# Kernel tuning notes

Measured on AMD Instinct MI355X. Metric: run time of the kernel, lower is better.

## Reference

```python
import jax, jax.numpy as jnp
import numpy as np

N, E, IN, ED, HID, HEADS, OUT, G = 50000, 800000, 128, 16, 32, 4, 64, 64
NEG_SLOPE = 0.2


def gat_conv(x, src, dst, edge_attr, W, att_src, att_dst, We, att_edge, bias,
             heads, out_ch, concat):
    """PyG-style GATConv with edge attributes and mean-filled self loops.
    src/dst already include self loops; edge_attr already includes fill rows."""
    n = x.shape[0]
    h = (x @ W).reshape(n, heads, out_ch)                      # [N,H,C]
    a_src = jnp.einsum('nhc,hc->nh', h, att_src)               # [N,H]
    a_dst = jnp.einsum('nhc,hc->nh', h, att_dst)
    eh = (edge_attr @ We).reshape(-1, heads, out_ch)           # [E',H,C]
    a_edge = jnp.einsum('ehc,hc->eh', eh, att_edge)            # [E',H]
    alpha = jax.nn.leaky_relu(a_src[src] + a_dst[dst] + a_edge, NEG_SLOPE)
    # segment softmax over incoming edges of each target node
    amax = jax.ops.segment_max(alpha, dst, num_segments=n)
    ex = jnp.exp(alpha - amax[dst])
    denom = jax.ops.segment_sum(ex, dst, num_segments=n)
    coef = ex / (denom[dst] + 1e-16)                           # [E',H]
    msg = h[src] * coef[:, :, None]                            # [E',H,C]
    out = jax.ops.segment_sum(msg, dst, num_segments=n)        # [N,H,C]
    out = out.reshape(n, heads * out_ch) if concat else out.mean(axis=1)
    return out + bias


def add_self_loops(edge_index, edge_attr, n):
    loop = jnp.arange(n, dtype=edge_index.dtype)
    src = jnp.concatenate([edge_index[0], loop])
    dst = jnp.concatenate([edge_index[1], loop])
    fill = jnp.broadcast_to(edge_attr.mean(axis=0), (n, edge_attr.shape[1]))
    ea = jnp.concatenate([edge_attr, fill], axis=0)
    return src, dst, ea


def setup_inputs() -> dict:
    key = jax.random.key(0)
    ks = jax.random.split(key, 16)
    s1 = 1.0 / np.sqrt(IN)
    s2 = 1.0 / np.sqrt(HID * HEADS)
    se = 1.0 / np.sqrt(ED)
    return {
        'x': jax.random.normal(ks[0], (N, IN), jnp.float32),
        'edge_index': jax.random.randint(ks[1], (2, E), 0, N, jnp.int64),
        'edge_attr': jax.random.normal(ks[2], (E, ED), jnp.float32),
        'batch': jnp.sort(jax.random.randint(ks[3], (N,), 0, G, jnp.int64)),
        # layer 1 params (heads=4, concat=True)
        'W1': jax.random.normal(ks[4], (IN, HEADS * HID), jnp.float32) * s1,
        'att_src1': jax.random.normal(ks[5], (HEADS, HID), jnp.float32) * s1,
        'att_dst1': jax.random.normal(ks[6], (HEADS, HID), jnp.float32) * s1,
        'We1': jax.random.normal(ks[7], (ED, HEADS * HID), jnp.float32) * se,
        'att_edge1': jax.random.normal(ks[8], (HEADS, HID), jnp.float32) * se,
        'b1': jnp.zeros((HEADS * HID,), jnp.float32),
        # layer 2 params (heads=1, concat=False)
        'W2': jax.random.normal(ks[9], (HEADS * HID, OUT), jnp.float32) * s2,
        'att_src2': jax.random.normal(ks[10], (1, OUT), jnp.float32) * s2,
        'att_dst2': jax.random.normal(ks[11], (1, OUT), jnp.float32) * s2,
        'We2': jax.random.normal(ks[12], (ED, OUT), jnp.float32) * se,
        'att_edge2': jax.random.normal(ks[13], (1, OUT), jnp.float32) * se,
        'b2': jnp.zeros((OUT,), jnp.float32),
    }


def reference(x, edge_index, edge_attr, batch,
              W1, att_src1, att_dst1, We1, att_edge1, b1,
              W2, att_src2, att_dst2, We2, att_edge2, b2):
    src, dst, ea = add_self_loops(edge_index, edge_attr, x.shape[0])
    h = gat_conv(x, src, dst, ea, W1, att_src1, att_dst1, We1, att_edge1, b1,
                 HEADS, HID, concat=True)
    h = jax.nn.elu(h)
    h = gat_conv(h, src, dst, ea, W2, att_src2, att_dst2, We2, att_edge2, b2,
                 1, OUT, concat=False)
    # global mean pool over graphs
    sums = jax.ops.segment_sum(h, batch, num_segments=G)
    cnts = jax.ops.segment_sum(jnp.ones((h.shape[0],), h.dtype), batch, num_segments=G)
    return sums / jnp.maximum(cnts, 1.0)[:, None]
```

## Files before the change

### kernel.cpp

```cpp
#include <hip/hip_runtime.h>
#include <hip/hip_fp16.h>
#include <math.h>

#define NN 50000
#define NE 800000
#define EDF 16
#define C1 128
#define HID 32
#define OUTF 64
#define NG 64
#define SLOPE 0.2f
#define CAP 64
#define PB 256
#define PCH 196
#define HB 3125
#define PRB 125
#define G2B 1563
#define FB 4688
#define ZTOT 54104
#define ZB 212
#define WZB 309

static inline int cdiv(long a, long b){ return (int)((a + b - 1) / b); }

__device__ __forceinline__ float lrelu(float x){ return x >= 0.f ? x : SLOPE * x; }

typedef _Float16 f16x8 __attribute__((ext_vector_type(8)));
typedef float f32x4 __attribute__((ext_vector_type(4)));
#define MFMA16(a, b, c) __builtin_amdgcn_mfma_f32_16x16x32_f16((a), (b), (c), 0, 0, 0)

__global__ __launch_bounds__(256) void k_wsplit(
    const float* __restrict__ W1, const float* __restrict__ W2,
    __half* __restrict__ W1Th, __half* __restrict__ W1Tl,
    __half* __restrict__ W2Th, __half* __restrict__ W2Tl,
    int* __restrict__ zbase,
    const float* __restrict__ We1, const float* __restrict__ att_e1,
    const float* __restrict__ We2, const float* __restrict__ att_e2,
    float* __restrict__ M1g, float* __restrict__ M2g){
  int t = threadIdx.x;
  int bid = blockIdx.x;
  if (bid < 64){
    int i = bid * 256 + t;
    int c = i & 127, k = i >> 7;
    float w = W1[i];
    __half h = __float2half_rn(w);
    W1Th[c * 128 + k] = h;
    W1Tl[c * 128 + k] = __float2half_rn((w - __half2float(h)) * 4096.0f);
    return;
  }
  if (bid < 96){
    int i = (bid - 64) * 256 + t;
    int c = i & 63, k = i >> 6;
    float w = W2[i];
    __half h = __float2half_rn(w);
    W2Th[c * 128 + k] = h;
    W2Tl[c * 128 + k] = __float2half_rn((w - __half2float(h)) * 4096.0f);
    return;
  }
  if (bid < 96 + ZB){
    int i = (bid - 96) * 256 + t;
    if (i < ZTOT) zbase[i] = 0;
    return;
  }
  if (t < 64){
    int h = t >> 4, d = t & 15;
    float s = 0.f;
    for (int c = 0; c < HID; c++) s += We1[d * C1 + h * HID + c] * att_e1[h * HID + c];
    M1g[t] = s;
  }
  if (t >= 64 && t < 80){
    int d = t - 64;
    float s = 0.f;
    for (int c = 0; c < OUTF; c++) s += We2[d * OUTF + c] * att_e2[c];
    M2g[d] = s;
  }
}

__global__ __launch_bounds__(256) void k_fuse(
    const float* __restrict__ ea,
    const int* __restrict__ src, const int* __restrict__ dst,
    const float* __restrict__ M1g, const float* __restrict__ M2g,
    int* __restrict__ deg, unsigned int* __restrict__ recC,
    float* __restrict__ part,
    const float* __restrict__ x,
    const __half* __restrict__ W1Th, const __half* __restrict__ W1Tl,
    __half* __restrict__ Ch,
    const float* __restrict__ attS, const float* __restrict__ attD,
    float* __restrict__ aS, float* __restrict__ aD){
  __shared__ __align__(16) __half Ash[4096];
  __shared__ __align__(16) __half Asl[4096];
  __shared__ float sM[80];
  __shared__ float sWS[64];
  int t = threadIdx.x;
  int bid = blockIdx.x;
  int rem = bid % 3;
  if (rem != 0){
    int pb = (bid / 3) * 2 + (rem - 1);
    if (t < 80) sM[t] = (t < 64) ? M1g[t] : M2g[t - 64];
    __syncthreads();
    long e = (long)pb * 256 + t;
    float eav[16];
    const float4* p = (const float4*)(ea + e * EDF);
    *(float4*)&eav[0]  = p[0]; *(float4*)&eav[4]  = p[1];
    *(float4*)&eav[8]  = p[2]; *(float4*)&eav[12] = p[3];
    int s = src[e];
    int d = dst[e];
    unsigned rk = (unsigned)atomicAdd(&deg[d], 1);
    float ae[4];
#pragma unroll
    for (int h = 0; h < 4; h++){
      float sdot = 0.f;
#pragma unroll
      for (int dd = 0; dd < 16; dd++) sdot += eav[dd] * sM[h * 16 + dd];
      ae[h] = sdot;
    }
    float a2 = 0.f;
#pragma unroll
    for (int dd = 0; dd < 16; dd++) a2 += eav[dd] * sM[64 + dd];
    __half2 ae01 = __floats2half2_rn(ae[0], ae[1]);
    __half2 ae23 = __floats2half2_rn(ae[2], ae[3]);
    __half  a2h  = __float2half_rn(a2);
    uint4 rec;
    rec.x = (unsigned)s | ((unsigned)*(unsigned short*)&a2h << 16);
    rec.y = *(unsigned*)&ae01;
    rec.z = *(unsigned*)&ae23;
    rec.w = 0u;
    *(uint4*)&recC[((long)d * CAP + rk) * 4] = rec;
    int lane = t & 63, wid = t >> 6;
#pragma unroll
    for (int c = 0; c < 16; c++){
      float v = eav[c];
#pragma unroll
      for (int off = 32; off > 0; off >>= 1) v += __shfl_xor(v, off);
      if (lane == 0) sWS[wid * 16 + c] = v;
    }
    __syncthreads();
    if (t < 16)
      part[pb * 16 + t] = sWS[t] + sWS[16 + t] + sWS[32 + t] + sWS[48 + t];
    return;
  }
  int row0 = (bid / 3) * 32;
  {
    int srow = t >> 3, sseg = t & 7;
    int gr = row0 + srow;
    float xv[16];
    if (gr < NN){
      const float4* xp = (const float4*)(x + (long)gr * 128 + sseg * 16);
      *(float4*)&xv[0]  = xp[0]; *(float4*)&xv[4]  = xp[1];
      *(float4*)&xv[8]  = xp[2]; *(float4*)&xv[12] = xp[3];
    } else {
#pragma unroll
      for (int i = 0; i < 16; i++) xv[i] = 0.f;
    }
    f16x8 vh[2], vl[2];
#pragma unroll
    for (int q = 0; q < 2; q++)
#pragma unroll
      for (int i = 0; i < 8; i++){
        float f = xv[q * 8 + i];
        _Float16 h = (_Float16)f;
        vh[q][i] = h;
        vl[q][i] = (_Float16)(f - (float)h);
      }
    int sb = srow * 256 + sseg * 32;
    int sw = (srow & 7) << 4;
    *(f16x8*)((char*)Ash + ((sb     ) ^ sw)) = vh[0];
    *(f16x8*)((char*)Ash + ((sb + 16) ^ sw)) = vh[1];
    *(f16x8*)((char*)Asl + ((sb     ) ^ sw)) = vl[0];
    *(f16x8*)((char*)Asl + ((sb + 16) ^ sw)) = vl[1];
  }
  __syncthreads();
  int wave = t >> 6, lane = t & 63, g = lane >> 4, li = lane & 15;
  const f16x8* BhP = (const f16x8*)W1Th;
  const f16x8* BlP = (const f16x8*)W1Tl;
  int c0 = wave * 32 + li;
  int c1 = c0 + 16;
  f32x4 z = {0.f, 0.f, 0.f, 0.f};
  f32x4 aM00 = z, aM01 = z, aM10 = z, aM11 = z;
  f32x4 aL00 = z, aL01 = z, aL10 = z, aL11 = z;
  int ro0 = li * 256, ro1 = (16 + li) * 256;
  int sw0 = (li & 7) << 4;
#pragma unroll
  for (int ks = 0; ks < 4; ks++){
    int ko = ks * 64 + g * 16;
    f16x8 ah0 = *(const f16x8*)((char*)Ash + ((ro0 + ko) ^ sw0));
    f16x8 ah1 = *(const f16x8*)((char*)Ash + ((ro1 + ko) ^ sw0));
    f16x8 al0 = *(const f16x8*)((char*)Asl + ((ro0 + ko) ^ sw0));
    f16x8 al1 = *(const f16x8*)((char*)Asl + ((ro1 + ko) ^ sw0));
    f16x8 bh0 = BhP[c0 * 16 + ks * 4 + g];
    f16x8 bh1 = BhP[c1 * 16 + ks * 4 + g];
    f16x8 bl0 = BlP[c0 * 16 + ks * 4 + g];
    f16x8 bl1 = BlP[c1 * 16 + ks * 4 + g];
    aM00 = MFMA16(ah0, bh0, aM00); aM01 = MFMA16(ah0, bh1, aM01);
    aM10 = MFMA16(ah1, bh0, aM10); aM11 = MFMA16(ah1, bh1, aM11);
    aM00 = MFMA16(al0, bh0, aM00); aM01 = MFMA16(al0, bh1, aM01);
    aM10 = MFMA16(al1, bh0, aM10); aM11 = MFMA16(al1, bh1, aM11);
    aL00 = MFMA16(ah0, bl0, aL00); aL01 = MFMA16(ah0, bl1, aL01);
    aL10 = MFMA16(ah1, bl0, aL10); aL11 = MFMA16(ah1, bl1, aL11);
  }
  const float s = 1.0f / 4096.0f;
  f32x4 D00 = aM00 + aL00 * s, D01 = aM01 + aL01 * s;
  f32x4 D10 = aM10 + aL10 * s, D11 = aM11 + aL11 * s;
  float avS0 = attS[c0], avS1 = attS[c1];
  float avD0 = attD[c0], avD1 = attD[c1];
  float ssv[2][4], sdv[2][4];
#pragma unroll
  for (int r = 0; r < 4; r++){
    ssv[0][r] = D00[r] * avS0 + D01[r] * avS1;
    ssv[1][r] = D10[r] * avS0 + D11[r] * avS1;
    sdv[0][r] = D00[r] * avD0 + D01[r] * avD1;
    sdv[1][r] = D10[r] * avD0 + D11[r] * avD1;
  }
#pragma unroll
  for (int off = 1; off <= 8; off <<= 1)
#pragma unroll
    for (int mt = 0; mt < 2; mt++)
#pragma unroll
      for (int r = 0; r < 4; r++){
        ssv[mt][r] += __shfl_xor(ssv[mt][r], off);
        sdv[mt][r] += __shfl_xor(sdv[mt][r], off);
      }
  __syncthreads();
  __half* sOut = Ash;
#pragma unroll
  for (int mt = 0; mt < 2; mt++)
#pragma unroll
    for (int r = 0; r < 4; r++){
      int rl = mt * 16 + g * 4 + r;
      sOut[rl * 128 + c0] = __float2half_rn(mt ? D10[r] : D00[r]);
      sOut[rl * 128 + c1] = __float2half_rn(mt ? D11[r] : D01[r]);
    }
  if (li == 0){
#pragma unroll
    for (int mt = 0; mt < 2; mt++)
#pragma unroll
      for (int r = 0; r < 4; r++){
        int grow = row0 + mt * 16 + g * 4 + r;
        if (grow < NN){
          aS[(long)grow * 4 + wave] = ssv[mt][r];
          aD[(long)grow * 4 + wave] = sdv[mt][r];
        }
      }
  }
  __syncthreads();
  {
    int row = t >> 3, seg = t & 7;
    int grw = row0 + row;
    if (grw < NN){
      uint4 u0 = *(uint4*)&sOut[row * 128 + seg * 16];
      uint4 u1 = *(uint4*)&sOut[row * 128 + seg * 16 + 8];
      *(uint4*)&Ch[(long)grw * 128 + seg * 16] = u0;
      *(uint4*)&Ch[(long)grw * 128 + seg * 16 + 8] = u1;
    }
  }
}

__global__ void k_red(const float* __restrict__ part, float* __restrict__ part2,
                      int* __restrict__ tick,
                      const float* __restrict__ M1g, const float* __restrict__ M2g,
                      float* __restrict__ aeSL1, float* __restrict__ aeSL2){
  int t = threadIdx.x;
  int j = blockIdx.x;
  __shared__ float red[256];
  __shared__ int isLast;
  int c = t & 15, r = t >> 4;
  int base = j * 25;
  float s0 = part[(base + r) * 16 + c];
  if (r < 9) s0 += part[(base + 16 + r) * 16 + c];
  red[t] = s0;
  __syncthreads();
  for (int st = 8; st >= 1; st >>= 1){
    if (r < st) red[t] += red[t + st * 16];
    __syncthreads();
  }
  if (r == 0) part2[j * 16 + c] = red[t];
  __syncthreads();
  if (t == 0){
    __threadfence();
    isLast = (atomicAdd(tick, 1) == PRB - 1);
  }
  __syncthreads();
  if (!isLast) return;
  __threadfence();
  __shared__ float sMean[16];
  {
    int q = t >> 4;
    float m0 = 0.f;
    for (int b = q; b < PRB; b += 16) m0 += part2[b * 16 + c];
    red[t] = m0;
  }
  __syncthreads();
  if (t < 16){
    float m = 0.f;
    for (int q2 = 0; q2 < 16; q2++) m += red[q2 * 16 + t];
    sMean[t] = m * (1.0f / NE);
  }
  __syncthreads();
  if (t < 4){
    float s = 0.f;
    for (int d = 0; d < 16; d++) s += sMean[d] * M1g[t * 16 + d];
    aeSL1[t] = s;
  }
  if (t == 4){
    float s = 0.f;
    for (int d = 0; d < 16; d++) s += sMean[d] * M2g[d];
    *aeSL2 = s;
  }
}

__global__ __launch_bounds__(256) void k_agg1(
    const int* __restrict__ deg, const unsigned int* __restrict__ recC,
    const float* __restrict__ a_src, const float* __restrict__ a_dst,
    const float* __restrict__ aeSL1,
    const __half* __restrict__ h1h, const float* __restrict__ b1,
    __half* __restrict__ out1h){
  __shared__ int   sS[4][CAP];
  __shared__ float sC[4][CAP * 4];
  int wid = threadIdx.x >> 6;
  int lane = threadIdx.x & 63;
  int n = blockIdx.x * 4 + wid;
  long start = (long)n * CAP;
  int dg = deg[n];
  float4 sl4 = *(const float4*)aeSL1;
  float4 ad4 = *(const float4*)(a_dst + (long)n * 4);
  float4 as4 = *(const float4*)(a_src + (long)n * 4);
  float4 cSelf;
  cSelf.x = __expf(lrelu(as4.x + ad4.x + sl4.x));
  cSelf.y = __expf(lrelu(as4.y + ad4.y + sl4.y));
  cSelf.z = __expf(lrelu(as4.z + ad4.z + sl4.z));
  cSelf.w = __expf(lrelu(as4.w + ad4.w + sl4.w));
  float4 dsum = make_float4(0.f, 0.f, 0.f, 0.f);
  {
    int j = lane;
    if (j < dg){
      uint4 rec = *(const uint4*)&recC[(start + j) * 4];
      int s = rec.x & 0xffff;
      float2 ae01 = __half22float2(*(__half2*)&rec.y);
      float2 ae23 = __half22float2(*(__half2*)&rec.z);
      float4 asv = *(const float4*)(a_src + (long)s * 4);
      float4 c;
      c.x = __expf(lrelu(asv.x + ad4.x + ae01.x));
      c.y = __expf(lrelu(asv.y + ad4.y + ae01.y));
      c.z = __expf(lrelu(asv.z + ad4.z + ae23.x));
      c.w = __expf(lrelu(asv.w + ad4.w + ae23.y));
      dsum.x = c.x; dsum.y = c.y; dsum.z = c.z; dsum.w = c.w;
      sS[wid][j] = s << 6;
      *(float4*)&sC[wid][j * 4] = c;
    }
  }
#pragma unroll
  for (int off = 32; off > 0; off >>= 1){
    dsum.x += __shfl_xor(dsum.x, off);
    dsum.y += __shfl_xor(dsum.y, off);
    dsum.z += __shfl_xor(dsum.z, off);
    dsum.w += __shfl_xor(dsum.w, off);
  }
  float csA[4] = {cSelf.x, cSelf.y, cSelf.z, cSelf.w};
  float invA[4];
  invA[0] = 1.f / (dsum.x + cSelf.x + 1e-16f);
  invA[1] = 1.f / (dsum.y + cSelf.y + 1e-16f);
  invA[2] = 1.f / (dsum.z + cSelf.z + 1e-16f);
  invA[3] = 1.f / (dsum.w + cSelf.w + 1e-16f);
  int ch = lane * 2;
  int h = lane >> 4;
  const unsigned int* hrow = (const unsigned int*)h1h;
  float cs   = csA[h];
  float vinv = invA[h];
  unsigned int hv = hrow[(unsigned)(n * 64 + lane)];
  float2 hf = __half22float2(*(__half2*)&hv);
  float acc0 = hf.x * cs, acc1 = hf.y * cs;
  int j = 0;
  for (; j + 4 <= dg; j += 4){
    int o0 = sS[wid][j+0], o1 = sS[wid][j+1], o2 = sS[wid][j+2], o3 = sS[wid][j+3];
    float c0 = sC[wid][(j+0)*4+h], c1 = sC[wid][(j+1)*4+h];
    float c2 = sC[wid][(j+2)*4+h], c3 = sC[wid][(j+3)*4+h];
    unsigned int v0 = hrow[(unsigned)(o0 + lane)];
    unsigned int v1 = hrow[(unsigned)(o1 + lane)];
    unsigned int v2 = hrow[(unsigned)(o2 + lane)];
    unsigned int v3 = hrow[(unsigned)(o3 + lane)];
    float2 f0 = __half22float2(*(__half2*)&v0);
    float2 f1 = __half22float2(*(__half2*)&v1);
    float2 f2 = __half22float2(*(__half2*)&v2);
    float2 f3 = __half22float2(*(__half2*)&v3);
    acc0 += c0 * f0.x + c1 * f1.x + c2 * f2.x + c3 * f3.x;
    acc1 += c0 * f0.y + c1 * f1.y + c2 * f2.y + c3 * f3.y;
  }
  for (; j < dg; j++){
    int o = sS[wid][j];
    float c = sC[wid][j * 4 + h];
    unsigned int v = hrow[(unsigned)(o + lane)];
    float2 f = __half22float2(*(__half2*)&v);
    acc0 += c * f.x; acc1 += c * f.y;
  }
  float v0 = acc0 * vinv + b1[ch];
  float v1 = acc1 * vinv + b1[ch + 1];
  v0 = v0 > 0.f ? v0 : __expf(v0) - 1.f;
  v1 = v1 > 0.f ? v1 : __expf(v1) - 1.f;
  __half2 pk = __floats2half2_rn(v0, v1);
  ((unsigned int*)out1h)[(unsigned)(n * 64 + lane)] = *(unsigned*)&pk;
}

__global__ __launch_bounds__(256) void k_agg2(
    const int* __restrict__ deg, const unsigned int* __restrict__ recC,
    const float* __restrict__ a_src, const float* __restrict__ a_dst,
    const float* __restrict__ aeSL2,
    const __half* __restrict__ h2h, float* __restrict__ out2){
  __shared__ int   sS[4][CAP];
  __shared__ float sC[4][CAP];
  int wid = threadIdx.x >> 6;
  int lane = threadIdx.x & 63;
  int n = blockIdx.x * 4 + wid;
  long start = (long)n * CAP;
  int dg = deg[n];
  float adN = a_dst[n];
  float cSelf = __expf(lrelu(a_src[n] + adN + *aeSL2));
  float dsum = 0.f;
  {
    int j = lane;
    if (j < dg){
      unsigned rx = recC[(start + j) * 4];
      int s = rx & 0xffff;
      unsigned short ah = (unsigned short)(rx >> 16);
      float c = __expf(lrelu(a_src[s] + adN + __half2float(*(__half*)&ah)));
      dsum = c;
      sS[wid][j] = s << 6; sC[wid][j] = c;
    }
  }
#pragma unroll
  for (int off = 32; off > 0; off >>= 1) dsum += __shfl_xor(dsum, off);
  float inv = 1.f / (dsum + cSelf + 1e-16f);
  float acc = __half2float(h2h[(unsigned)(n * 64 + lane)]) * cSelf;
  int j = 0;
  for (; j + 4 <= dg; j += 4){
    int o0 = sS[wid][j+0], o1 = sS[wid][j+1], o2 = sS[wid][j+2], o3 = sS[wid][j+3];
    float c0 = sC[wid][j+0], c1 = sC[wid][j+1], c2 = sC[wid][j+2], c3 = sC[wid][j+3];
    float f0 = __half2float(h2h[(unsigned)(o0 + lane)]);
    float f1 = __half2float(h2h[(unsigned)(o1 + lane)]);
    float f2 = __half2float(h2h[(unsigned)(o2 + lane)]);
    float f3 = __half2float(h2h[(unsigned)(o3 + lane)]);
    acc += c0 * f0 + c1 * f1 + c2 * f2 + c3 * f3;
  }
  for (; j < dg; j++)
    acc += sC[wid][j] * __half2float(h2h[(unsigned)(sS[wid][j] + lane)]);
  out2[(long)n * OUTF + lane] = acc * inv;
}

__global__ __launch_bounds__(256) void k_gemm2(
    const __half* __restrict__ Ahp,
    const __half* __restrict__ W2Th, const __half* __restrict__ W2Tl,
    __half* __restrict__ Ch,
    const float* __restrict__ attS, const float* __restrict__ attD,
    float* __restrict__ aS, float* __restrict__ aD){
  __shared__ __align__(16) __half As[4096];
  __shared__ float sRS[128], sRD[128];
  int t = threadIdx.x;
  int row0 = blockIdx.x * 32;
  {
    int srow = t >> 3, sseg = t & 7;
    int gr = row0 + srow;
    uint4 u0 = {0,0,0,0}, u1 = {0,0,0,0};
    if (gr < NN){
      const uint4* p = (const uint4*)(Ahp + (long)gr * 128 + sseg * 16);
      u0 = p[0]; u1 = p[1];
    }
    int sb = srow * 256 + sseg * 32;
    int sw = (srow & 7) << 4;
    *(uint4*)((char*)As + ((sb     ) ^ sw)) = u0;
    *(uint4*)((char*)As + ((sb + 16) ^ sw)) = u1;
  }
  __syncthreads();
  int wave = t >> 6, lane = t & 63, g = lane >> 4, li = lane & 15;
  int cw = wave * 16 + li;
  const f16x8* BhP = (const f16x8*)W2Th;
  const f16x8* BlP = (const f16x8*)W2Tl;
  f32x4 z = {0.f, 0.f, 0.f, 0.f};
  f32x4 aM0 = z, aM1 = z, aL0 = z, aL1 = z;
  int ro0 = li * 256, ro1 = (16 + li) * 256, sw0 = (li & 7) << 4;
#pragma unroll
  for (int ks = 0; ks < 4; ks++){
    int ko = ks * 64 + g * 16;
    f16x8 a0 = *(const f16x8*)((char*)As + ((ro0 + ko) ^ sw0));
    f16x8 a1 = *(const f16x8*)((char*)As + ((ro1 + ko) ^ sw0));
    f16x8 bh = BhP[cw * 16 + ks * 4 + g];
    f16x8 bl = BlP[cw * 16 + ks * 4 + g];
    aM0 = MFMA16(a0, bh, aM0); aM1 = MFMA16(a1, bh, aM1);
    aL0 = MFMA16(a0, bl, aL0); aL1 = MFMA16(a1, bl, aL1);
  }
  const float s = 1.0f / 4096.0f;
  f32x4 D0 = aM0 + aL0 * s, D1 = aM1 + aL1 * s;
  float avS = attS[cw], avD = attD[cw];
  float ssv[2][4], sdv[2][4];
#pragma unroll
  for (int r = 0; r < 4; r++){
    ssv[0][r] = D0[r] * avS; ssv[1][r] = D1[r] * avS;
    sdv[0][r] = D0[r] * avD; sdv[1][r] = D1[r] * avD;
  }
#pragma unroll
  for (int off = 1; off <= 8; off <<= 1)
#pragma unroll
    for (int mt = 0; mt < 2; mt++)
#pragma unroll
      for (int r = 0; r < 4; r++){
        ssv[mt][r] += __shfl_xor(ssv[mt][r], off);
        sdv[mt][r] += __shfl_xor(sdv[mt][r], off);
      }
  __syncthreads();
  __half* sOut = As;
#pragma unroll
  for (int mt = 0; mt < 2; mt++)
#pragma unroll
    for (int r = 0; r < 4; r++){
      int rl = mt * 16 + g * 4 + r;
      sOut[rl * 64 + cw] = __float2half_rn(mt ? D1[r] : D0[r]);
      if (li == 0){
        sRS[wave * 32 + rl] = ssv[mt][r];
        sRD[wave * 32 + rl] = sdv[mt][r];
      }
    }
  __syncthreads();
  if (t < 32){
    int grow = row0 + t;
    if (grow < NN){
      aS[grow] = sRS[t] + sRS[32 + t] + sRS[64 + t] + sRS[96 + t];
      aD[grow] = sRD[t] + sRD[32 + t] + sRD[64 + t] + sRD[96 + t];
    }
  }
  {
    int row = t >> 3, seg = t & 7;
    int grw = row0 + row;
    if (grw < NN)
      *(uint4*)&Ch[(long)grw * 64 + seg * 8] = *(uint4*)&sOut[row * 64 + seg * 8];
  }
}

__global__ __launch_bounds__(256) void k_pool(const float* __restrict__ out2,
                                              const int* __restrict__ batch,
                                              float* __restrict__ gsum,
                                              int* __restrict__ tick,
                                              const float* __restrict__ b2,
                                              float* __restrict__ out){
  int t = threadIdx.x;
  int c = t & 63, r = t >> 6;
  int n0 = blockIdx.x * PCH + r;
  int n1 = blockIdx.x * PCH + PCH; if (n1 > NN) n1 = NN;
  float acc = 0.f; int curG = -1;
  for (int n = n0; n < n1; n += 4){
    int g = batch[n];
    if (g != curG){
      if (curG >= 0) atomicAdd(&gsum[curG * 64 + c], acc);
      curG = g; acc = 0.f;
    }
    acc += out2[(long)n * OUTF + c];
  }
  if (curG >= 0) atomicAdd(&gsum[curG * 64 + c], acc);
  __shared__ int isLast;
  __shared__ int sCnt[64];
  __syncthreads();
  if (t == 0){
    __threadfence();
    isLast = (atomicAdd(tick, 1) == PB - 1);
  }
  __syncthreads();
  if (!isLast) return;
  __threadfence();
  if (t < 64){
    int g = t;
    int lo = 0, hi = NN;
    while (lo < hi){ int mid = (lo + hi) >> 1; if (batch[mid] < g) lo = mid + 1; else hi = mid; }
    int a = lo, b = NN;
    while (a < b){ int mid = (a + b) >> 1; if (batch[mid] < g + 1) a = mid + 1; else b = mid; }
    sCnt[g] = a - lo;
  }
  __syncthreads();
#pragma unroll
  for (int k = 0; k < 16; k++){
    int i = t + k * 256;
    int g = i >> 6, cc = i & 63;
    float cnt = (float)sCnt[g];
    out[i] = (gsum[i] + cnt * b2[cc]) / fmaxf(cnt, 1.0f);
  }
}

extern "C" void kernel_launch(void* const* d_in, const int* in_sizes, int n_in,
                              void* d_out, int out_size, void* d_ws, size_t ws_size,
                              hipStream_t stream) {
  const float* x         = (const float*)d_in[0];
  const int*   eidx      = (const int*)d_in[1];
  const float* edge_attr = (const float*)d_in[2];
  const int*   batch     = (const int*)d_in[3];
  const float* W1        = (const float*)d_in[4];
  const float* att_src1  = (const float*)d_in[5];
  const float* att_dst1  = (const float*)d_in[6];
  const float* We1       = (const float*)d_in[7];
  const float* att_edge1 = (const float*)d_in[8];
  const float* b1        = (const float*)d_in[9];
  const float* W2        = (const float*)d_in[10];
  const float* att_src2  = (const float*)d_in[11];
  const float* att_dst2  = (const float*)d_in[12];
  const float* We2       = (const float*)d_in[13];
  const float* att_edge2 = (const float*)d_in[14];
  const float* b2        = (const float*)d_in[15];
  const int* srcI = eidx;
  const int* dstI = eidx + NE;

  float* ws = (float*)d_ws;
  __half* h1h   = (__half*)ws;
  __half* out1h = (__half*)(ws + 3200000);
  float* out2   = ws + 6400000;
  float* a_src1 = ws + 9600000;
  float* a_dst1 = a_src1 + (long)NN * 4;
  unsigned int* recC = (unsigned int*)(a_dst1 + (long)NN * 4);
  int*   deg    = (int*)(recC + (long)NN * CAP * 4);
  float* gsum   = (float*)(deg + NN);
  int*   tick   = (int*)(gsum + NG * 64);
  float* part   = (float*)(tick + 8);
  float* part2  = part + (long)HB * 16;
  float* aeSL1  = part2 + (long)PRB * 16;
  float* aeSL2  = aeSL1 + 4;
  float* M1g    = aeSL2 + 4;
  float* M2g    = M1g + 64;
  __half* W1Th  = (__half*)(M2g + 16);
  __half* W1Tl  = W1Th + 16384;
  __half* W2Th  = W1Tl + 16384;
  __half* W2Tl  = W2Th + 8192;
  __half* h2h = h1h;
  float* a_src2 = a_src1; float* a_dst2 = a_dst1;

  k_wsplit<<<WZB, 256, 0, stream>>>(W1, W2, W1Th, W1Tl, W2Th, W2Tl,
                                    deg,
                                    We1, att_edge1, We2, att_edge2,
                                    M1g, M2g);
  k_fuse<<<FB, 256, 0, stream>>>(edge_attr, srcI, dstI, M1g, M2g,
                                 deg, recC, part,
                                 x, W1Th, W1Tl, h1h, att_src1, att_dst1,
                                 a_src1, a_dst1);
  k_red<<<PRB, 256, 0, stream>>>(part, part2, &tick[0], M1g, M2g, aeSL1, aeSL2);
  k_agg1<<<NN / 4, 256, 0, stream>>>(deg, recC, a_src1, a_dst1, aeSL1,
                                     h1h, b1, out1h);
  k_gemm2<<<G2B, 256, 0, stream>>>(out1h, W2Th, W2Tl, h2h, att_src2, att_dst2,
                                   a_src2, a_dst2);
  k_agg2<<<NN / 4, 256, 0, stream>>>(deg, recC, a_src2, a_dst2, aeSL2,
                                     h2h, out2);
  k_pool<<<PB, 256, 0, stream>>>(out2, batch, gsum, &tick[1], b2, (float*)d_out);
}
```

Before: 293.7 us.

## Fuse layer-2 linear transform and attention logits into layer-1 aggregation kernel

Measured after the change: 344.2 us. 17.2% more time.

```diff
diff --git a/kernel.cpp b/kernel.cpp
--- a/kernel.cpp
+++ b/kernel.cpp
@@ -15,11 +15,10 @@
 #define PCH 196
 #define HB 3125
 #define PRB 125
-#define G2B 1563
 #define FB 4688
 #define ZTOT 54104
 #define ZB 212
-#define WZB 309
+#define WZB 277
 
 static inline int cdiv(long a, long b){ return (int)((a + b - 1) / b); }
 
@@ -30,9 +29,8 @@
 #define MFMA16(a, b, c) __builtin_amdgcn_mfma_f32_16x16x32_f16((a), (b), (c), 0, 0, 0)
 
 __global__ __launch_bounds__(256) void k_wsplit(
-    const float* __restrict__ W1, const float* __restrict__ W2,
+    const float* __restrict__ W1,
     __half* __restrict__ W1Th, __half* __restrict__ W1Tl,
-    __half* __restrict__ W2Th, __half* __restrict__ W2Tl,
     int* __restrict__ zbase,
     const float* __restrict__ We1, const float* __restrict__ att_e1,
     const float* __restrict__ We2, const float* __restrict__ att_e2,
@@ -48,17 +46,8 @@
     W1Tl[c * 128 + k] = __float2half_rn((w - __half2float(h)) * 4096.0f);
     return;
   }
-  if (bid < 96){
+  if (bid < 64 + ZB){
     int i = (bid - 64) * 256 + t;
-    int c = i & 63, k = i >> 6;
-    float w = W2[i];
-    __half h = __float2half_rn(w);
-    W2Th[c * 128 + k] = h;
-    W2Tl[c * 128 + k] = __float2half_rn((w - __half2float(h)) * 4096.0f);
-    return;
-  }
-  if (bid < 96 + ZB){
-    int i = (bid - 96) * 256 + t;
     if (i < ZTOT) zbase[i] = 0;
     return;
   }
@@ -313,7 +302,9 @@
     const float* __restrict__ a_src, const float* __restrict__ a_dst,
     const float* __restrict__ aeSL1,
     const __half* __restrict__ h1h, const float* __restrict__ b1,
-    __half* __restrict__ out1h){
+    const float* __restrict__ W2,
+    const float* __restrict__ attS2, const float* __restrict__ attD2,
+    __half* __restrict__ h2out, float* __restrict__ aS2, float* __restrict__ aD2){
   __shared__ int   sS[4][CAP];
   __shared__ float sC[4][CAP * 4];
   int wid = threadIdx.x >> 6;
@@ -396,8 +387,24 @@
   float v1 = acc1 * vinv + b1[ch + 1];
   v0 = v0 > 0.f ? v0 : __expf(v0) - 1.f;
   v1 = v1 > 0.f ? v1 : __expf(v1) - 1.f;
-  __half2 pk = __floats2half2_rn(v0, v1);
-  ((unsigned int*)out1h)[(unsigned)(n * 64 + lane)] = *(unsigned*)&pk;
+  float p0 = 0.f, p1 = 0.f;
+#pragma unroll 8
+  for (int k2 = 0; k2 < 64; k2++){
+    float r0 = __shfl(v0, k2);
+    float r1 = __shfl(v1, k2);
+    p0 += r0 * W2[(k2 * 2) * 64 + lane];
+    p1 += r1 * W2[(k2 * 2 + 1) * 64 + lane];
+  }
+  float h2v = p0 + p1;
+  h2out[(unsigned)(n * 64 + lane)] = __float2half_rn(h2v);
+  float s2 = h2v * attS2[lane];
+  float d2 = h2v * attD2[lane];
+#pragma unroll
+  for (int off = 1; off <= 32; off <<= 1){
+    s2 += __shfl_xor(s2, off);
+    d2 += __shfl_xor(d2, off);
+  }
+  if (lane == 0){ aS2[n] = s2; aD2[n] = d2; }
 }
 
 __global__ __launch_bounds__(256) void k_agg2(
@@ -445,94 +452,6 @@
   out2[(long)n * OUTF + lane] = acc * inv;
 }
 
-__global__ __launch_bounds__(256) void k_gemm2(
-    const __half* __restrict__ Ahp,
-    const __half* __restrict__ W2Th, const __half* __restrict__ W2Tl,
-    __half* __restrict__ Ch,
-    const float* __restrict__ attS, const float* __restrict__ attD,
-    float* __restrict__ aS, float* __restrict__ aD){
-  __shared__ __align__(16) __half As[4096];
-  __shared__ float sRS[128], sRD[128];
-  int t = threadIdx.x;
-  int row0 = blockIdx.x * 32;
-  {
-    int srow = t >> 3, sseg = t & 7;
-    int gr = row0 + srow;
-    uint4 u0 = {0,0,0,0}, u1 = {0,0,0,0};
-    if (gr < NN){
-      const uint4* p = (const uint4*)(Ahp + (long)gr * 128 + sseg * 16);
-      u0 = p[0]; u1 = p[1];
-    }
-    int sb = srow * 256 + sseg * 32;
-    int sw = (srow & 7) << 4;
-    *(uint4*)((char*)As + ((sb     ) ^ sw)) = u0;
-    *(uint4*)((char*)As + ((sb + 16) ^ sw)) = u1;
-  }
-  __syncthreads();
-  int wave = t >> 6, lane = t & 63, g = lane >> 4, li = lane & 15;
-  int cw = wave * 16 + li;
-  const f16x8* BhP = (const f16x8*)W2Th;
-  const f16x8* BlP = (const f16x8*)W2Tl;
-  f32x4 z = {0.f, 0.f, 0.f, 0.f};
-  f32x4 aM0 = z, aM1 = z, aL0 = z, aL1 = z;
-  int ro0 = li * 256, ro1 = (16 + li) * 256, sw0 = (li & 7) << 4;
-#pragma unroll
-  for (int ks = 0; ks < 4; ks++){
-    int ko = ks * 64 + g * 16;
-    f16x8 a0 = *(const f16x8*)((char*)As + ((ro0 + ko) ^ sw0));
-    f16x8 a1 = *(const f16x8*)((char*)As + ((ro1 + ko) ^ sw0));
-    f16x8 bh = BhP[cw * 16 + ks * 4 + g];
-    f16x8 bl = BlP[cw * 16 + ks * 4 + g];
-    aM0 = MFMA16(a0, bh, aM0); aM1 = MFMA16(a1, bh, aM1);
-    aL0 = MFMA16(a0, bl, aL0); aL1 = MFMA16(a1, bl, aL1);
-  }
-  const float s = 1.0f / 4096.0f;
-  f32x4 D0 = aM0 + aL0 * s, D1 = aM1 + aL1 * s;
-  float avS = attS[cw], avD = attD[cw];
-  float ssv[2][4], sdv[2][4];
-#pragma unroll
-  for (int r = 0; r < 4; r++){
-    ssv[0][r] = D0[r] * avS; ssv[1][r] = D1[r] * avS;
-    sdv[0][r] = D0[r] * avD; sdv[1][r] = D1[r] * avD;
-  }
-#pragma unroll
-  for (int off = 1; off <= 8; off <<= 1)
-#pragma unroll
-    for (int mt = 0; mt < 2; mt++)
-#pragma unroll
-      for (int r = 0; r < 4; r++){
-        ssv[mt][r] += __shfl_xor(ssv[mt][r], off);
-        sdv[mt][r] += __shfl_xor(sdv[mt][r], off);
-      }
-  __syncthreads();
-  __half* sOut = As;
-#pragma unroll
-  for (int mt = 0; mt < 2; mt++)
-#pragma unroll
-    for (int r = 0; r < 4; r++){
-      int rl = mt * 16 + g * 4 + r;
-      sOut[rl * 64 + cw] = __float2half_rn(mt ? D1[r] : D0[r]);
-      if (li == 0){
-        sRS[wave * 32 + rl] = ssv[mt][r];
-        sRD[wave * 32 + rl] = sdv[mt][r];
-      }
-    }
-  __syncthreads();
-  if (t < 32){
-    int grow = row0 + t;
-    if (grow < NN){
-      aS[grow] = sRS[t] + sRS[32 + t] + sRS[64 + t] + sRS[96 + t];
-      aD[grow] = sRD[t] + sRD[32 + t] + sRD[64 + t] + sRD[96 + t];
-    }
-  }
-  {
-    int row = t >> 3, seg = t & 7;
-    int grw = row0 + row;
-    if (grw < NN)
-      *(uint4*)&Ch[(long)grw * 64 + seg * 8] = *(uint4*)&sOut[row * 64 + seg * 8];
-  }
-}
-
 __global__ __launch_bounds__(256) void k_pool(const float* __restrict__ out2,
                                               const int* __restrict__ batch,
                                               float* __restrict__ gsum,
@@ -605,11 +524,13 @@
 
   float* ws = (float*)d_ws;
   __half* h1h   = (__half*)ws;
-  __half* out1h = (__half*)(ws + 3200000);
+  __half* h2out = (__half*)(ws + 3200000);
   float* out2   = ws + 6400000;
   float* a_src1 = ws + 9600000;
   float* a_dst1 = a_src1 + (long)NN * 4;
-  unsigned int* recC = (unsigned int*)(a_dst1 + (long)NN * 4);
+  float* aS2    = a_dst1 + (long)NN * 4;
+  float* aD2    = aS2 + NN;
+  unsigned int* recC = (unsigned int*)(aD2 + NN);
   int*   deg    = (int*)(recC + (long)NN * CAP * 4);
   float* gsum   = (float*)(deg + NN);
   int*   tick   = (int*)(gsum + NG * 64);
@@ -621,12 +542,8 @@
   float* M2g    = M1g + 64;
   __half* W1Th  = (__half*)(M2g + 16);
   __half* W1Tl  = W1Th + 16384;
-  __half* W2Th  = W1Tl + 16384;
-  __half* W2Tl  = W2Th + 8192;
-  __half* h2h = h1h;
-  float* a_src2 = a_src1; float* a_dst2 = a_dst1;
-
-  k_wsplit<<<WZB, 256, 0, stream>>>(W1, W2, W1Th, W1Tl, W2Th, W2Tl,
+
+  k_wsplit<<<WZB, 256, 0, stream>>>(W1, W1Th, W1Tl,
                                     deg,
                                     We1, att_edge1, We2, att_edge2,
                                     M1g, M2g);
@@ -636,10 +553,10 @@
                                  a_src1, a_dst1);
   k_red<<<PRB, 256, 0, stream>>>(part, part2, &tick[0], M1g, M2g, aeSL1, aeSL2);
   k_agg1<<<NN / 4, 256, 0, stream>>>(deg, recC, a_src1, a_dst1, aeSL1,
-                                     h1h, b1, out1h);
-  k_gemm2<<<G2B, 256, 0, stream>>>(out1h, W2Th, W2Tl, h2h, att_src2, att_dst2,
-                                   a_src2, a_dst2);
-  k_agg2<<<NN / 4, 256, 0, stream>>>(deg, recC, a_src2, a_dst2, aeSL2,
-                                     h2h, out2);
+                                     h1h, b1,
+                                     W2, att_src2, att_dst2,
+                                     h2out, aS2, aD2);
+  k_agg2<<<NN / 4, 256, 0, stream>>>(deg, recC, aS2, aD2, aeSL2,
+                                     h2out, out2);
   k_pool<<<PB, 256, 0, stream>>>(out2, batch, gsum, &tick[1], b2, (float*)d_out);
 }
```

## Fuse layer-1 aggregation with layer-2 GEMM via shared-memory tile

Applied to the files above, without the earlier changes.

After: 313.0 us. 6.6% more time.

```diff
diff --git a/kernel.cpp b/kernel.cpp
--- a/kernel.cpp
+++ b/kernel.cpp
@@ -15,7 +15,7 @@
 #define PCH 196
 #define HB 3125
 #define PRB 125
-#define G2B 1563
+#define AGB 1563
 #define FB 4688
 #define ZTOT 54104
 #define ZB 212
@@ -308,96 +308,175 @@
   }
 }
 
-__global__ __launch_bounds__(256) void k_agg1(
+__global__ __launch_bounds__(512) void k_agg1(
     const int* __restrict__ deg, const unsigned int* __restrict__ recC,
     const float* __restrict__ a_src, const float* __restrict__ a_dst,
     const float* __restrict__ aeSL1,
     const __half* __restrict__ h1h, const float* __restrict__ b1,
-    __half* __restrict__ out1h){
-  __shared__ int   sS[4][CAP];
-  __shared__ float sC[4][CAP * 4];
-  int wid = threadIdx.x >> 6;
-  int lane = threadIdx.x & 63;
-  int n = blockIdx.x * 4 + wid;
-  long start = (long)n * CAP;
-  int dg = deg[n];
-  float4 sl4 = *(const float4*)aeSL1;
-  float4 ad4 = *(const float4*)(a_dst + (long)n * 4);
-  float4 as4 = *(const float4*)(a_src + (long)n * 4);
-  float4 cSelf;
-  cSelf.x = __expf(lrelu(as4.x + ad4.x + sl4.x));
-  cSelf.y = __expf(lrelu(as4.y + ad4.y + sl4.y));
-  cSelf.z = __expf(lrelu(as4.z + ad4.z + sl4.z));
-  cSelf.w = __expf(lrelu(as4.w + ad4.w + sl4.w));
-  float4 dsum = make_float4(0.f, 0.f, 0.f, 0.f);
-  {
-    int j = lane;
-    if (j < dg){
-      uint4 rec = *(const uint4*)&recC[(start + j) * 4];
-      int s = rec.x & 0xffff;
-      float2 ae01 = __half22float2(*(__half2*)&rec.y);
-      float2 ae23 = __half22float2(*(__half2*)&rec.z);
-      float4 asv = *(const float4*)(a_src + (long)s * 4);
-      float4 c;
-      c.x = __expf(lrelu(asv.x + ad4.x + ae01.x));
-      c.y = __expf(lrelu(asv.y + ad4.y + ae01.y));
-      c.z = __expf(lrelu(asv.z + ad4.z + ae23.x));
-      c.w = __expf(lrelu(asv.w + ad4.w + ae23.y));
-      dsum.x = c.x; dsum.y = c.y; dsum.z = c.z; dsum.w = c.w;
-      sS[wid][j] = s << 6;
-      *(float4*)&sC[wid][j * 4] = c;
-    }
-  }
-#pragma unroll
-  for (int off = 32; off > 0; off >>= 1){
-    dsum.x += __shfl_xor(dsum.x, off);
-    dsum.y += __shfl_xor(dsum.y, off);
-    dsum.z += __shfl_xor(dsum.z, off);
-    dsum.w += __shfl_xor(dsum.w, off);
-  }
-  float csA[4] = {cSelf.x, cSelf.y, cSelf.z, cSelf.w};
-  float invA[4];
-  invA[0] = 1.f / (dsum.x + cSelf.x + 1e-16f);
-  invA[1] = 1.f / (dsum.y + cSelf.y + 1e-16f);
-  invA[2] = 1.f / (dsum.z + cSelf.z + 1e-16f);
-  invA[3] = 1.f / (dsum.w + cSelf.w + 1e-16f);
-  int ch = lane * 2;
-  int h = lane >> 4;
+    const __half* __restrict__ W2Th, const __half* __restrict__ W2Tl,
+    const float* __restrict__ attS2, const float* __restrict__ attD2,
+    __half* __restrict__ h2h, float* __restrict__ aS2, float* __restrict__ aD2){
+  __shared__ int   sS[8][CAP];
+  __shared__ float sC[8][CAP * 4];
+  __shared__ __align__(16) __half As[4096];
+  __shared__ float sRS[128], sRD[128];
+  int t = threadIdx.x;
+  int wid = t >> 6;
+  int lane = t & 63;
+  int nb = blockIdx.x * 32;
   const unsigned int* hrow = (const unsigned int*)h1h;
-  float cs   = csA[h];
-  float vinv = invA[h];
-  unsigned int hv = hrow[(unsigned)(n * 64 + lane)];
-  float2 hf = __half22float2(*(__half2*)&hv);
-  float acc0 = hf.x * cs, acc1 = hf.y * cs;
-  int j = 0;
-  for (; j + 4 <= dg; j += 4){
-    int o0 = sS[wid][j+0], o1 = sS[wid][j+1], o2 = sS[wid][j+2], o3 = sS[wid][j+3];
-    float c0 = sC[wid][(j+0)*4+h], c1 = sC[wid][(j+1)*4+h];
-    float c2 = sC[wid][(j+2)*4+h], c3 = sC[wid][(j+3)*4+h];
-    unsigned int v0 = hrow[(unsigned)(o0 + lane)];
-    unsigned int v1 = hrow[(unsigned)(o1 + lane)];
-    unsigned int v2 = hrow[(unsigned)(o2 + lane)];
-    unsigned int v3 = hrow[(unsigned)(o3 + lane)];
-    float2 f0 = __half22float2(*(__half2*)&v0);
-    float2 f1 = __half22float2(*(__half2*)&v1);
-    float2 f2 = __half22float2(*(__half2*)&v2);
-    float2 f3 = __half22float2(*(__half2*)&v3);
-    acc0 += c0 * f0.x + c1 * f1.x + c2 * f2.x + c3 * f3.x;
-    acc1 += c0 * f0.y + c1 * f1.y + c2 * f2.y + c3 * f3.y;
-  }
-  for (; j < dg; j++){
-    int o = sS[wid][j];
-    float c = sC[wid][j * 4 + h];
-    unsigned int v = hrow[(unsigned)(o + lane)];
-    float2 f = __half22float2(*(__half2*)&v);
-    acc0 += c * f.x; acc1 += c * f.y;
-  }
-  float v0 = acc0 * vinv + b1[ch];
-  float v1 = acc1 * vinv + b1[ch + 1];
-  v0 = v0 > 0.f ? v0 : __expf(v0) - 1.f;
-  v1 = v1 > 0.f ? v1 : __expf(v1) - 1.f;
-  __half2 pk = __floats2half2_rn(v0, v1);
-  ((unsigned int*)out1h)[(unsigned)(n * 64 + lane)] = *(unsigned*)&pk;
+  for (int q = 0; q < 4; q++){
+    int n = nb + wid * 4 + q;
+    if (n < NN){
+      long start = (long)n * CAP;
+      int dg = deg[n];
+      float4 sl4 = *(const float4*)aeSL1;
+      float4 ad4 = *(const float4*)(a_dst + (long)n * 4);
+      float4 as4 = *(const float4*)(a_src + (long)n * 4);
+      float4 cSelf;
+      cSelf.x = __expf(lrelu(as4.x + ad4.x + sl4.x));
+      cSelf.y = __expf(lrelu(as4.y + ad4.y + sl4.y));
+      cSelf.z = __expf(lrelu(as4.z + ad4.z + sl4.z));
+      cSelf.w = __expf(lrelu(as4.w + ad4.w + sl4.w));
+      float4 dsum = make_float4(0.f, 0.f, 0.f, 0.f);
+      {
+        int j = lane;
+        if (j < dg){
+          uint4 rec = *(const uint4*)&recC[(start + j) * 4];
+          int s = rec.x & 0xffff;
+          float2 ae01 = __half22float2(*(__half2*)&rec.y);
+          float2 ae23 = __half22float2(*(__half2*)&rec.z);
+          float4 asv = *(const float4*)(a_src + (long)s * 4);
+          float4 c;
+          c.x = __expf(lrelu(asv.x + ad4.x + ae01.x));
+          c.y = __expf(lrelu(asv.y + ad4.y + ae01.y));
+          c.z = __expf(lrelu(asv.z + ad4.z + ae23.x));
+          c.w = __expf(lrelu(asv.w + ad4.w + ae23.y));
+          dsum.x = c.x; dsum.y = c.y; dsum.z = c.z; dsum.w = c.w;
+          sS[wid][j] = s << 6;
+          *(float4*)&sC[wid][j * 4] = c;
+        }
+      }
+#pragma unroll
+      for (int off = 32; off > 0; off >>= 1){
+        dsum.x += __shfl_xor(dsum.x, off);
+        dsum.y += __shfl_xor(dsum.y, off);
+        dsum.z += __shfl_xor(dsum.z, off);
+        dsum.w += __shfl_xor(dsum.w, off);
+      }
+      float csA[4] = {cSelf.x, cSelf.y, cSelf.z, cSelf.w};
+      float invA[4];
+      invA[0] = 1.f / (dsum.x + cSelf.x + 1e-16f);
+      invA[1] = 1.f / (dsum.y + cSelf.y + 1e-16f);
+      invA[2] = 1.f / (dsum.z + cSelf.z + 1e-16f);
+      invA[3] = 1.f / (dsum.w + cSelf.w + 1e-16f);
+      int ch = lane * 2;
+      int h = lane >> 4;
+      float cs   = csA[h];
+      float vinv = invA[h];
+      unsigned int hv = hrow[(unsigned)(n * 64 + lane)];
+      float2 hf = __half22float2(*(__half2*)&hv);
+      float acc0 = hf.x * cs, acc1 = hf.y * cs;
+      int j = 0;
+      for (; j + 4 <= dg; j += 4){
+        int o0 = sS[wid][j+0], o1 = sS[wid][j+1], o2 = sS[wid][j+2], o3 = sS[wid][j+3];
+        float c0 = sC[wid][(j+0)*4+h], c1 = sC[wid][(j+1)*4+h];
+        float c2 = sC[wid][(j+2)*4+h], c3 = sC[wid][(j+3)*4+h];
+        unsigned int v0 = hrow[(unsigned)(o0 + lane)];
+        unsigned int v1 = hrow[(unsigned)(o1 + lane)];
+        unsigned int v2 = hrow[(unsigned)(o2 + lane)];
+        unsigned int v3 = hrow[(unsigned)(o3 + lane)];
+        float2 f0 = __half22float2(*(__half2*)&v0);
+        float2 f1 = __half22float2(*(__half2*)&v1);
+        float2 f2 = __half22float2(*(__half2*)&v2);
+        float2 f3 = __half22float2(*(__half2*)&v3);
+        acc0 += c0 * f0.x + c1 * f1.x + c2 * f2.x + c3 * f3.x;
+        acc1 += c0 * f0.y + c1 * f1.y + c2 * f2.y + c3 * f3.y;
+      }
+      for (; j < dg; j++){
+        int o = sS[wid][j];
+        float c = sC[wid][j * 4 + h];
+        unsigned int v = hrow[(unsigned)(o + lane)];
+        float2 f = __half22float2(*(__half2*)&v);
+        acc0 += c * f.x; acc1 += c * f.y;
+      }
+      float v0 = acc0 * vinv + b1[ch];
+      float v1 = acc1 * vinv + b1[ch + 1];
+      v0 = v0 > 0.f ? v0 : __expf(v0) - 1.f;
+      v1 = v1 > 0.f ? v1 : __expf(v1) - 1.f;
+      int rl = wid * 4 + q;
+      int off = (rl * 256 + lane * 4) ^ ((rl & 7) << 4);
+      *(__half2*)((char*)As + off) = __floats2half2_rn(v0, v1);
+    }
+  }
+  __syncthreads();
+  f32x4 D0, D1;
+  float ssv[2][4], sdv[2][4];
+  int g = lane >> 4, li = lane & 15;
+  int cw = wid * 16 + li;
+  if (wid < 4){
+    const f16x8* BhP = (const f16x8*)W2Th;
+    const f16x8* BlP = (const f16x8*)W2Tl;
+    f32x4 z = {0.f, 0.f, 0.f, 0.f};
+    f32x4 aM0 = z, aM1 = z, aL0 = z, aL1 = z;
+    int ro0 = li * 256, ro1 = (16 + li) * 256, sw0 = (li & 7) << 4;
+#pragma unroll
+    for (int ks = 0; ks < 4; ks++){
+      int ko = ks * 64 + g * 16;
+      f16x8 a0 = *(const f16x8*)((char*)As + ((ro0 + ko) ^ sw0));
+      f16x8 a1 = *(const f16x8*)((char*)As + ((ro1 + ko) ^ sw0));
+      f16x8 bh = BhP[cw * 16 + ks * 4 + g];
+      f16x8 bl = BlP[cw * 16 + ks * 4 + g];
+      aM0 = MFMA16(a0, bh, aM0); aM1 = MFMA16(a1, bh, aM1);
+      aL0 = MFMA16(a0, bl, aL0); aL1 = MFMA16(a1, bl, aL1);
+    }
+    const float s = 1.0f / 4096.0f;
+    D0 = aM0 + aL0 * s; D1 = aM1 + aL1 * s;
+    float avS = attS2[cw], avD = attD2[cw];
+#pragma unroll
+    for (int r = 0; r < 4; r++){
+      ssv[0][r] = D0[r] * avS; ssv[1][r] = D1[r] * avS;
+      sdv[0][r] = D0[r] * avD; sdv[1][r] = D1[r] * avD;
+    }
+#pragma unroll
+    for (int off = 1; off <= 8; off <<= 1)
+#pragma unroll
+      for (int mt = 0; mt < 2; mt++)
+#pragma unroll
+        for (int r = 0; r < 4; r++){
+          ssv[mt][r] += __shfl_xor(ssv[mt][r], off);
+          sdv[mt][r] += __shfl_xor(sdv[mt][r], off);
+        }
+  }
+  __syncthreads();
+  __half* sOut = As;
+  if (wid < 4){
+#pragma unroll
+    for (int mt = 0; mt < 2; mt++)
+#pragma unroll
+      for (int r = 0; r < 4; r++){
+        int rl = mt * 16 + g * 4 + r;
+        sOut[rl * 64 + cw] = __float2half_rn(mt ? D1[r] : D0[r]);
+        if (li == 0){
+          sRS[wid * 32 + rl] = ssv[mt][r];
+          sRD[wid * 32 + rl] = sdv[mt][r];
+        }
+      }
+  }
+  __syncthreads();
+  if (t < 32){
+    int grow = nb + t;
+    if (grow < NN){
+      aS2[grow] = sRS[t] + sRS[32 + t] + sRS[64 + t] + sRS[96 + t];
+      aD2[grow] = sRD[t] + sRD[32 + t] + sRD[64 + t] + sRD[96 + t];
+    }
+  }
+  if (t < 256){
+    int row = t >> 3, seg = t & 7;
+    int grw = nb + row;
+    if (grw < NN)
+      *(uint4*)&h2h[(long)grw * 64 + seg * 8] = *(uint4*)&sOut[row * 64 + seg * 8];
+  }
 }
 
 __global__ __launch_bounds__(256) void k_agg2(
@@ -445,94 +524,6 @@
   out2[(long)n * OUTF + lane] = acc * inv;
 }
 
-__global__ __launch_bounds__(256) void k_gemm2(
-    const __half* __restrict__ Ahp,
-    const __half* __restrict__ W2Th, const __half* __restrict__ W2Tl,
-    __half* __restrict__ Ch,
-    const float* __restrict__ attS, const float* __restrict__ attD,
-    float* __restrict__ aS, float* __restrict__ aD){
-  __shared__ __align__(16) __half As[4096];
-  __shared__ float sRS[128], sRD[128];
-  int t = threadIdx.x;
-  int row0 = blockIdx.x * 32;
-  {
-    int srow = t >> 3, sseg = t & 7;
-    int gr = row0 + srow;
-    uint4 u0 = {0,0,0,0}, u1 = {0,0,0,0};
-    if (gr < NN){
-      const uint4* p = (const uint4*)(Ahp + (long)gr * 128 + sseg * 16);
-      u0 = p[0]; u1 = p[1];
-    }
-    int sb = srow * 256 + sseg * 32;
-    int sw = (srow & 7) << 4;
-    *(uint4*)((char*)As + ((sb     ) ^ sw)) = u0;
-    *(uint4*)((char*)As + ((sb + 16) ^ sw)) = u1;
-  }
-  __syncthreads();
-  int wave = t >> 6, lane = t & 63, g = lane >> 4, li = lane & 15;
-  int cw = wave * 16 + li;
-  const f16x8* BhP = (const f16x8*)W2Th;
-  const f16x8* BlP = (const f16x8*)W2Tl;
-  f32x4 z = {0.f, 0.f, 0.f, 0.f};
-  f32x4 aM0 = z, aM1 = z, aL0 = z, aL1 = z;
-  int ro0 = li * 256, ro1 = (16 + li) * 256, sw0 = (li & 7) << 4;
-#pragma unroll
-  for (int ks = 0; ks < 4; ks++){
-    int ko = ks * 64 + g * 16;
-    f16x8 a0 = *(const f16x8*)((char*)As + ((ro0 + ko) ^ sw0));
-    f16x8 a1 = *(const f16x8*)((char*)As + ((ro1 + ko) ^ sw0));
-    f16x8 bh = BhP[cw * 16 + ks * 4 + g];
-    f16x8 bl = BlP[cw * 16 + ks * 4 + g];
-    aM0 = MFMA16(a0, bh, aM0); aM1 = MFMA16(a1, bh, aM1);
-    aL0 = MFMA16(a0, bl, aL0); aL1 = MFMA16(a1, bl, aL1);
-  }
-  const float s = 1.0f / 4096.0f;
-  f32x4 D0 = aM0 + aL0 * s, D1 = aM1 + aL1 * s;
-  float avS = attS[cw], avD = attD[cw];
-  float ssv[2][4], sdv[2][4];
-#pragma unroll
-  for (int r = 0; r < 4; r++){
-    ssv[0][r] = D0[r] * avS; ssv[1][r] = D1[r] * avS;
-    sdv[0][r] = D0[r] * avD; sdv[1][r] = D1[r] * avD;
-  }
-#pragma unroll
-  for (int off = 1; off <= 8; off <<= 1)
-#pragma unroll
-    for (int mt = 0; mt < 2; mt++)
-#pragma unroll
-      for (int r = 0; r < 4; r++){
-        ssv[mt][r] += __shfl_xor(ssv[mt][r], off);
-        sdv[mt][r] += __shfl_xor(sdv[mt][r], off);
-      }
-  __syncthreads();
-  __half* sOut = As;
-#pragma unroll
-  for (int mt = 0; mt < 2; mt++)
-#pragma unroll
-    for (int r = 0; r < 4; r++){
-      int rl = mt * 16 + g * 4 + r;
-      sOut[rl * 64 + cw] = __float2half_rn(mt ? D1[r] : D0[r]);
-      if (li == 0){
-        sRS[wave * 32 + rl] = ssv[mt][r];
-        sRD[wave * 32 + rl] = sdv[mt][r];
-      }
-    }
-  __syncthreads();
-  if (t < 32){
-    int grow = row0 + t;
-    if (grow < NN){
-      aS[grow] = sRS[t] + sRS[32 + t] + sRS[64 + t] + sRS[96 + t];
-      aD[grow] = sRD[t] + sRD[32 + t] + sRD[64 + t] + sRD[96 + t];
-    }
-  }
-  {
-    int row = t >> 3, seg = t & 7;
-    int grw = row0 + row;
-    if (grw < NN)
-      *(uint4*)&Ch[(long)grw * 64 + seg * 8] = *(uint4*)&sOut[row * 64 + seg * 8];
-  }
-}
-
 __global__ __launch_bounds__(256) void k_pool(const float* __restrict__ out2,
                                               const int* __restrict__ batch,
                                               float* __restrict__ gsum,
@@ -605,11 +596,13 @@
 
   float* ws = (float*)d_ws;
   __half* h1h   = (__half*)ws;
-  __half* out1h = (__half*)(ws + 3200000);
+  __half* h2h   = (__half*)(ws + 3200000);
   float* out2   = ws + 6400000;
   float* a_src1 = ws + 9600000;
   float* a_dst1 = a_src1 + (long)NN * 4;
-  unsigned int* recC = (unsigned int*)(a_dst1 + (long)NN * 4);
+  float* aS2    = a_dst1 + (long)NN * 4;
+  float* aD2    = aS2 + NN;
+  unsigned int* recC = (unsigned int*)(aD2 + NN);
   int*   deg    = (int*)(recC + (long)NN * CAP * 4);
   float* gsum   = (float*)(deg + NN);
   int*   tick   = (int*)(gsum + NG * 64);
@@ -623,8 +616,6 @@
   __half* W1Tl  = W1Th + 16384;
   __half* W2Th  = W1Tl + 16384;
   __half* W2Tl  = W2Th + 8192;
-  __half* h2h = h1h;
-  float* a_src2 = a_src1; float* a_dst2 = a_dst1;
 
   k_wsplit<<<WZB, 256, 0, stream>>>(W1, W2, W1Th, W1Tl, W2Th, W2Tl,
                                     deg,
@@ -635,11 +626,11 @@
                                  x, W1Th, W1Tl, h1h, att_src1, att_dst1,
                                  a_src1, a_dst1);
   k_red<<<PRB, 256, 0, stream>>>(part, part2, &tick[0], M1g, M2g, aeSL1, aeSL2);
-  k_agg1<<<NN / 4, 256, 0, stream>>>(deg, recC, a_src1, a_dst1, aeSL1,
-                                     h1h, b1, out1h);
-  k_gemm2<<<G2B, 256, 0, stream>>>(out1h, W2Th, W2Tl, h2h, att_src2, att_dst2,
-                                   a_src2, a_dst2);
-  k_agg2<<<NN / 4, 256, 0, stream>>>(deg, recC, a_src2, a_dst2, aeSL2,
+  k_agg1<<<AGB, 512, 0, stream>>>(deg, recC, a_src1, a_dst1, aeSL1,
+                                  h1h, b1,
+                                  W2Th, W2Tl, att_src2, att_dst2,
+                                  h2h, aS2, aD2);
+  k_agg2<<<NN / 4, 256, 0, stream>>>(deg, recC, aS2, aD2, aeSL2,
                                      h2h, out2);
   k_pool<<<PB, 256, 0, stream>>>(out2, batch, gsum, &tick[1], b2, (float*)d_out);
 }
```
